# Kernel tuning notes

Measured on AMD Instinct MI355X. Metric: run time of the kernel, lower is better.

Reference implementation:

```python
import jax, jax.numpy as jnp
import numpy as np

B, N, F, E, D, H, L = 4, 2048, 2, 16, 32, 4, 2
GRAPH_LAYERS = 3
FLOW_ITERS = 10
COST_C = 1.0        # quadratic cost: c*x^2, inv_derivative(y) = y/(2c)
BIG_NUMBER = 1e7


def setup_inputs():
    key = jax.random.key(0)
    ks = jax.random.split(key, 20)
    node_features = jax.random.normal(ks[0], (B, N, F), jnp.float32)
    node_embeddings = jax.random.normal(ks[1], (B, N, E), jnp.float32)
    demands = jax.random.normal(ks[2], (B, N, 1), jnp.float32)
    demands = demands - demands.mean(axis=1, keepdims=True)  # flow conservation
    adj = (jax.random.uniform(ks[3], (B, N, N)) < 0.01).astype(jnp.float32)
    adj = adj * (1.0 - jnp.eye(N, dtype=jnp.float32))
    eye = jnp.broadcast_to(jnp.eye(N, dtype=jnp.float32), (B, N, N))
    neighborhoods = jnp.stack([eye, adj], axis=1)  # [B,L,N,N] hop-0 and hop-1
    def g(k, shape):
        return jax.random.normal(k, shape, jnp.float32) * 0.1
    params = {
        'We1': g(ks[4], (E + F, D)), 'be1': jnp.zeros((D,), jnp.float32),
        'We2': g(ks[5], (D, D)), 'be2': jnp.zeros((D,), jnp.float32),
        'w_attn': g(ks[6], (H, D)),
        'Wo': g(ks[7], (D, D)), 'bo': jnp.zeros((D,), jnp.float32),
        'Wz': g(ks[8], (D, D)), 'Uz': g(ks[9], (D, D)), 'bz': jnp.zeros((D,), jnp.float32),
        'Wr': g(ks[10], (D, D)), 'Ur': g(ks[11], (D, D)), 'br': jnp.zeros((D,), jnp.float32),
        'Wh': g(ks[12], (D, D)), 'Uh': g(ks[13], (D, D)), 'bh': jnp.zeros((D,), jnp.float32),
        'Wd1': g(ks[14], (D, D)), 'bd1': jnp.zeros((D,), jnp.float32),
        'Wd2': g(ks[15], (D, 1)), 'bd2': jnp.zeros((1,), jnp.float32),
        'Wv1': g(ks[16], (D, D)), 'bv1': jnp.zeros((D,), jnp.float32),
        'Wv2': g(ks[17], (D, 1)), 'bv2': jnp.zeros((1,), jnp.float32),
    }
    return {'node_features': node_features, 'node_embeddings': node_embeddings,
            'demands': demands, 'adj': adj, 'neighborhoods': neighborhoods, **params}


def _forward(node_features, node_embeddings, demands, adj, neighborhoods,
             We1, be1, We2, be2, w_attn, Wo, bo,
             Wz, Uz, bz, Wr, Ur, br, Wh, Uh, bh,
             Wd1, bd1, Wd2, bd2, Wv1, bv1, Wv2, bv2):
    # --- node encoder MLP (tanh, activate_final=True) ---
    x = jnp.concatenate([node_embeddings, node_features], axis=-1)   # [B,N,E+F]
    enc = jnp.tanh(jnp.tanh(x @ We1 + be1) @ We2 + be2)               # [B,N,D]
    # row-normalized neighborhood operators (degree-normalized aggregation)
    Mnorm = neighborhoods / (jnp.sum(neighborhoods, axis=-1, keepdims=True) + 1.0)
    # --- graph_layers x (attention neighborhood + GRU state update) ---
    for _ in range(GRAPH_LAYERS):
        agg = jnp.einsum('blnm,bmd->blnd', Mnorm, enc)                # [B,L,N,D]
        scores = jnp.einsum('blnd,hd->bhnl', jnp.tanh(agg), w_attn)   # [B,H,N,L]
        alpha = jax.nn.softmax(scores, axis=-1)
        ctx = jnp.einsum('bhnl,blnd->bnd', alpha, agg) / H            # mean over heads
        nbr = jnp.tanh(ctx @ Wo + bo)                                 # [B,N,D]
        z = jax.nn.sigmoid(nbr @ Wz + enc @ Uz + bz)
        r = jax.nn.sigmoid(nbr @ Wr + enc @ Ur + br)
        h = jnp.tanh(nbr @ Wh + (r * enc) @ Uh + bh)
        enc = z * enc + (1.0 - z) * h
    # --- primal: edge weights, masked softmax, proportional flow solver ---
    pred = (enc @ Wd1 + bd1) @ Wd2 + bd2                              # [B,N,1]
    pw = pred * jnp.transpose(pred, (0, 2, 1))                        # [B,N,N]
    weights = -BIG_NUMBER * (1.0 - adj) + pw
    fwp = jax.nn.softmax(weights, axis=-1)                            # rows sum to 1
    flow0 = fwp * jax.nn.relu(-demands)

    def step(flow, _):
        inflow = jnp.sum(flow, axis=1)[..., None]                     # [B,N,1]
        return fwp * jax.nn.relu(inflow - demands), None

    flow, _ = jax.lax.scan(step, flow0, None, length=FLOW_ITERS)
    flow_cost = jnp.sum(COST_C * flow * flow, axis=(1, 2))            # [B]
    # --- dual: dual variables, dual flows via inverse cost derivative ---
    dual = (enc @ Wv1 + bv1) @ Wv2 + bv2                              # [B,N,1]
    dd = dual - jnp.transpose(dual, (0, 2, 1))                        # [B,N,N]
    df = adj * jax.nn.relu(dd / (2.0 * COST_C))
    dual_cost = jnp.sum(COST_C * df * df - dd * df, axis=(1, 2)) \
        - jnp.sum(dual * demands, axis=(1, 2))                        # [B]
    return flow_cost - dual_cost                                      # primal-dual gap loss, [B]


def reference(node_features, node_embeddings, demands, adj, neighborhoods,
              We1, be1, We2, be2, w_attn, Wo, bo,
              Wz, Uz, bz, Wr, Ur, br, Wh, Uh, bh,
              Wd1, bd1, Wd2, bd2, Wv1, bv1, Wv2, bv2):
    return _forward(node_features, node_embeddings, demands, adj, neighborhoods,
                    We1, be1, We2, be2, w_attn, Wo, bo,
                    Wz, Uz, bz, Wr, Ur, br, Wh, Uh, bh,
                    Wd1, bd1, Wd2, bd2, Wv1, bv1, Wv2, bv2)
```

## Files before the change

kernel.cpp:

```cpp
#include <hip/hip_runtime.h>

#define NN 2048
#define NB 4
#define BN (NB * NN)
#define MAXD 96

__device__ __forceinline__ float fast_rcp(float x) { return __builtin_amdgcn_rcpf(x); }
__device__ __forceinline__ float fast_tanh(float x) {
    float a = __expf(2.0f * fabsf(x));
    float r = 1.0f - 2.0f * fast_rcp(1.0f + a);
    return copysignf(r, x);
}
__device__ __forceinline__ float fast_sigmoid(float x) {
    return fast_rcp(1.0f + __expf(-x));
}

__global__ __launch_bounds__(256) void k_front(
    const float* __restrict__ feat, const float* __restrict__ emb,
    const float* __restrict__ We1, const float* __restrict__ be1,
    const float* __restrict__ We2, const float* __restrict__ be2,
    float* __restrict__ enc_out,
    const float* __restrict__ adj, int* __restrict__ deg, int* __restrict__ cols,
    int* __restrict__ tdeg)
{
    int tid = threadIdx.x;
    if (blockIdx.x < 1024) {
        __shared__ float sW1[18 * 32], sb1[32], sW2[32 * 32], sb2[32];
        for (int i = tid; i < 18 * 32; i += 256) sW1[i] = We1[i];
        for (int i = tid; i < 32 * 32; i += 256) sW2[i] = We2[i];
        if (tid < 32) { sb1[tid] = be1[tid]; sb2[tid] = be2[tid]; }
        __syncthreads();
        int group = tid >> 5, j = tid & 31;
        int node = blockIdx.x * 8 + group;
        float x;
        if (j < 16)      x = emb[node * 16 + j];
        else if (j < 18) x = feat[node * 2 + (j - 16)];
        else             x = 0.f;
        float acc = sb1[j];
#pragma unroll
        for (int k = 0; k < 18; k++)
            acc += __shfl(x, k, 32) * sW1[k * 32 + j];
        float h = fast_tanh(acc);
        float acc2 = sb2[j];
#pragma unroll
        for (int k = 0; k < 32; k++)
            acc2 += __shfl(h, k, 32) * sW2[k * 32 + j];
        enc_out[node * 32 + j] = fast_tanh(acc2);
    } else {
        int wave = tid >> 6, lane = tid & 63;
        int row = (blockIdx.x - 1024) * 4 + wave;
        const float4* p = (const float4*)(adj + (size_t)row * NN);
        int cnt = 0;
        int base = row * MAXD;
#pragma unroll
        for (int it = 0; it < 8; it++) {
            float4 v = p[it * 64 + lane];
            float va[4] = { v.x, v.y, v.z, v.w };
#pragma unroll
            for (int c = 0; c < 4; c++) {
                unsigned long long m = __ballot(va[c] != 0.f);
                if (va[c] != 0.f) {
                    int pos = cnt + __popcll(m & ((1ull << lane) - 1ull));
                    if (pos < MAXD) cols[base + pos] = it * 256 + lane * 4 + c;
                }
                cnt += __popcll(m);
            }
        }
        if (lane == 0) {
            deg[row] = cnt < MAXD ? cnt : MAXD;
            tdeg[row] = 0;
        }
    }
}

__global__ __launch_bounds__(1024) void k_perm(
    const int* __restrict__ deg, const int* __restrict__ cols,
    int* __restrict__ perm, int* __restrict__ rank, int* __restrict__ degS)
{
    __shared__ int sIndeg[NN];
    __shared__ int sHist[MAXD + 1];
    __shared__ int sOff[MAXD + 1];
    int tid = threadIdx.x, b = blockIdx.x;
    for (int n = tid; n < NN; n += 1024) sIndeg[n] = 0;
    if (tid <= MAXD) sHist[tid] = 0;
    __syncthreads();
    for (int r = tid; r < NN; r += 1024) {
        int row = b * NN + r;
        int d = deg[row];
        const int* cp = cols + row * MAXD;
        for (int i = 0; i < d; i++) atomicAdd(&sIndeg[cp[i]], 1);
    }
    __syncthreads();
    for (int n = tid; n < NN; n += 1024) {
        int dg = sIndeg[n]; if (dg > MAXD) dg = MAXD;
        sIndeg[n] = dg;
        atomicAdd(&sHist[dg], 1);
    }
    __syncthreads();
    if (tid == 0) {
        int acc = 0;
        for (int i = 0; i <= MAXD; i++) { sOff[i] = acc; acc += sHist[i]; }
    }
    __syncthreads();
    for (int n = tid; n < NN; n += 1024) {
        int dg = sIndeg[n];
        int r = atomicAdd(&sOff[dg], 1);
        perm[b * NN + r] = n;
        rank[b * NN + n] = r;
        degS[b * NN + r] = dg;
    }
}

__device__ __forceinline__ float layer_rest(
    int g, int j, float e, float a1raw, int d,
    const float4* sPack, const float2* sWhUh, const float* sWo,
    const float* sAttn, const float* sbo, const float* sbz,
    const float* sbr, const float* sbh,
    float2 (*sNE)[32], float (*sCtx)[32])
{
    float agg0 = 0.5f * e;
    float a1 = a1raw * fast_rcp((float)(d + 1));
    float t0 = fast_tanh(agg0), t1 = fast_tanh(a1);
    float td = t0 - t1;
    float s0 = sAttn[j] * td, s1 = sAttn[32 + j] * td,
          s2 = sAttn[64 + j] * td, s3 = sAttn[96 + j] * td;
#pragma unroll
    for (int off = 16; off >= 1; off >>= 1) {
        s0 += __shfl_xor(s0, off, 32);
        s1 += __shfl_xor(s1, off, 32);
        s2 += __shfl_xor(s2, off, 32);
        s3 += __shfl_xor(s3, off, 32);
    }
    float c0 = 0.25f * (fast_sigmoid(s0) + fast_sigmoid(s1) +
                        fast_sigmoid(s2) + fast_sigmoid(s3));
    float ctx = c0 * agg0 + (1.0f - c0) * a1;
    sCtx[g][j] = ctx;
    float acc = sbo[j];
#pragma unroll
    for (int k = 0; k < 32; k += 2) {
        float2 c2 = *(const float2*)&sCtx[g][k];
        acc += c2.x * sWo[k * 32 + j] + c2.y * sWo[(k + 1) * 32 + j];
    }
    float nbr = fast_tanh(acc);
    sNE[g][j] = make_float2(nbr, e);
    float az = sbz[j], ar = sbr[j];
#pragma unroll
    for (int k = 0; k < 32; k += 2) {
        float4 ne2 = *(const float4*)&sNE[g][k];
        float4 w0  = sPack[k * 32 + j];
        float4 w1  = sPack[(k + 1) * 32 + j];
        az += ne2.x * w0.x + ne2.y * w0.y + ne2.z * w1.x + ne2.w * w1.y;
        ar += ne2.x * w0.z + ne2.y * w0.w + ne2.z * w1.z + ne2.w * w1.w;
    }
    float z = fast_sigmoid(az), r = fast_sigmoid(ar);
    sNE[g][j].y = r * e;
    float ah = sbh[j];
#pragma unroll
    for (int k = 0; k < 32; k += 2) {
        float4 ne2 = *(const float4*)&sNE[g][k];
        float2 w0 = sWhUh[k * 32 + j];
        float2 w1 = sWhUh[(k + 1) * 32 + j];
        ah += ne2.x * w0.x + ne2.y * w0.y + ne2.z * w1.x + ne2.w * w1.y;
    }
    float hc = fast_tanh(ah);
    return z * e + (1.0f - z) * hc;
}

__device__ __forceinline__ float hop1_gather(
    int g, int j, int d, const int* __restrict__ cp,
    const float* __restrict__ encB, int (*sCols)[64])
{
    sCols[g][j]      = cp[j];
    sCols[g][j + 32] = cp[j + 32];
    float a = 0.f, b = 0.f, c = 0.f, e4 = 0.f;
    int i = 0;
    for (; i + 3 < d; i += 4) {
        int m0 = sCols[g][i],     m1 = sCols[g][i + 1];
        int m2 = sCols[g][i + 2], m3 = sCols[g][i + 3];
        a  += encB[m0 * 32 + j];
        b  += encB[m1 * 32 + j];
        c  += encB[m2 * 32 + j];
        e4 += encB[m3 * 32 + j];
    }
    for (; i < d; i++) a += encB[sCols[g][i] * 32 + j];
    return (a + b) + (c + e4);
}

__global__ __launch_bounds__(1024) void k_layer(
    const float* __restrict__ enc_in, float* __restrict__ enc_out,
    const int* __restrict__ deg, const int* __restrict__ cols,
    const float* __restrict__ w_attn,
    const float* __restrict__ Wo, const float* __restrict__ bo,
    const float* __restrict__ Wz, const float* __restrict__ Uz, const float* __restrict__ bz,
    const float* __restrict__ Wr, const float* __restrict__ Ur, const float* __restrict__ br,
    const float* __restrict__ Wh, const float* __restrict__ Uh, const float* __restrict__ bh)
{
    __shared__ float4 sPack[1024];
    __shared__ float2 sWhUh[1024];
    __shared__ float  sWo[1024];
    __shared__ float  sAttn[128], sbo[32], sbz[32], sbr[32], sbh[32];
    __shared__ int    sCols[32][64];
    __shared__ __align__(16) float2 sNE[32][32];
    __shared__ __align__(16) float  sCtx[32][32];
    int tid = threadIdx.x;
    sPack[tid] = make_float4(Wz[tid], Uz[tid], Wr[tid], Ur[tid]);
    sWhUh[tid] = make_float2(Wh[tid], Uh[tid]);
    sWo[tid] = Wo[tid];
    if (tid < 128) sAttn[tid] = w_attn[tid];
    if (tid < 32) { sbo[tid] = bo[tid]; sbz[tid] = bz[tid]; sbr[tid] = br[tid]; sbh[tid] = bh[tid]; }
    int g = tid >> 5, j = tid & 31;
    int node = blockIdx.x * 32 + g;
    int b = node >> 11;
    const float* encB = enc_in + (size_t)(b * NN) * 32;
    float e = enc_in[node * 32 + j];
    int d = deg[node];
    const int* cp = cols + node * MAXD;
    float a1 = hop1_gather(g, j, d, cp, encB, sCols);
    __syncthreads();
    float eo = layer_rest(g, j, e, a1, d, sPack, sWhUh, sWo,
                          sAttn, sbo, sbz, sbr, sbh, sNE, sCtx);
    enc_out[node * 32 + j] = eo;
}

__global__ __launch_bounds__(1024) void k_layer_last(
    const float* __restrict__ enc_in,
    const int* __restrict__ deg, const int* __restrict__ cols,
    const float* __restrict__ w_attn,
    const float* __restrict__ Wo, const float* __restrict__ bo,
    const float* __restrict__ Wz, const float* __restrict__ Uz, const float* __restrict__ bz,
    const float* __restrict__ Wr, const float* __restrict__ Ur, const float* __restrict__ br,
    const float* __restrict__ Wh, const float* __restrict__ Uh, const float* __restrict__ bh,
    const float* __restrict__ Wd1, const float* __restrict__ bd1,
    const float* __restrict__ Wd2, const float* __restrict__ bd2,
    const float* __restrict__ Wv1, const float* __restrict__ bv1,
    const float* __restrict__ Wv2, const float* __restrict__ bv2,
    float* __restrict__ pred, float* __restrict__ dual)
{
    __shared__ float4 sPack[1024];
    __shared__ float2 sWhUh[1024];
    __shared__ float  sWo[1024];
    __shared__ float  sAttn[128], sbo[32], sbz[32], sbr[32], sbh[32];
    __shared__ float  swd[32], swv[32], shc[2];
    __shared__ int    sCols[32][64];
    __shared__ __align__(16) float2 sNE[32][32];
    __shared__ __align__(16) float  sCtx[32][32];
    int tid = threadIdx.x;
    sPack[tid] = make_float4(Wz[tid], Uz[tid], Wr[tid], Ur[tid]);
    sWhUh[tid] = make_float2(Wh[tid], Uh[tid]);
    sWo[tid] = Wo[tid];
    if (tid < 128) sAttn[tid] = w_attn[tid];
    if (tid < 32) { sbo[tid] = bo[tid]; sbz[tid] = bz[tid]; sbr[tid] = br[tid]; sbh[tid] = bh[tid]; }
    if (tid >= 64 && tid < 96) {
        int k = tid - 64;
        float a = 0.f, av = 0.f;
#pragma unroll
        for (int jj = 0; jj < 32; jj++) {
            a  += Wd1[k * 32 + jj] * Wd2[jj];
            av += Wv1[k * 32 + jj] * Wv2[jj];
        }
        swd[k] = a; swv[k] = av;
    }
    if (tid == 96) {
        float c1 = 0.f, c2 = 0.f;
#pragma unroll
        for (int jj = 0; jj < 32; jj++) {
            c1 += bd1[jj] * Wd2[jj];
            c2 += bv1[jj] * Wv2[jj];
        }
        shc[0] = c1 + bd2[0]; shc[1] = c2 + bv2[0];
    }
    int g = tid >> 5, j = tid & 31;
    int node = blockIdx.x * 32 + g;
    int b = node >> 11;
    const float* encB = enc_in + (size_t)(b * NN) * 32;
    float e = enc_in[node * 32 + j];
    int d = deg[node];
    const int* cp = cols + node * MAXD;
    float a1 = hop1_gather(g, j, d, cp, encB, sCols);
    __syncthreads();
    float eo = layer_rest(g, j, e, a1, d, sPack, sWhUh, sWo,
                          sAttn, sbo, sbz, sbr, sbh, sNE, sCtx);
    float pd = eo * swd[j];
    float dv = eo * swv[j];
#pragma unroll
    for (int off = 16; off >= 1; off >>= 1) {
        pd += __shfl_xor(pd, off, 32);
        dv += __shfl_xor(dv, off, 32);
    }
    if (j == 0) {
        pred[node] = pd + shc[0];
        dual[node] = dv + shc[1];
    }
}

__global__ __launch_bounds__(256) void k_edge_scatter(
    const int* __restrict__ deg, const int* __restrict__ cols,
    const float* __restrict__ pred, const float* __restrict__ dual,
    const int* __restrict__ rank,
    int* __restrict__ tdeg, unsigned* __restrict__ tpack,
    float* __restrict__ rowsq, float* __restrict__ rowdual)
{
    int wave = threadIdx.x >> 6, lane = threadIdx.x & 63;
    int row = blockIdx.x * 4 + wave;
    int b = row >> 11;
    int rloc = row & (NN - 1);
    const float* predB = pred + b * NN;
    const float* dualB = dual + b * NN;
    int d = deg[row];
    int base = row * MAXD;
    float pn = pred[row];
    float dn = dual[row];
    if (d <= 64) {
        int c = 0;
        float w = -1e30f, du = 0.f;
        bool act = lane < d;
        if (act) {
            c = cols[base + lane];
            w = pn * predB[c];
            float dd = dn - dualB[c];
            if (dd > 0.f) du = -0.25f * dd * dd;
        }
        float mx = w;
#pragma unroll
        for (int off = 32; off >= 1; off >>= 1) mx = fmaxf(mx, __shfl_xor(mx, off));
        float ex = act ? __expf(w - mx) : 0.f;
        float den = ex;
#pragma unroll
        for (int off = 32; off >= 1; off >>= 1) { den += __shfl_xor(den, off); du += __shfl_xor(du, off); }
        float f = ex * fast_rcp(den);
        float rs = f * f;
        if (act) {
            int pos = atomicAdd(&tdeg[b * NN + c], 1);
            if (pos < MAXD) {
                int rk = rank[b * NN + c];
                unsigned wv = ((__float_as_uint(f) + 0x400u) & 0xFFFFF800u) | (unsigned)rloc;
                tpack[(size_t)(b * MAXD + pos) * NN + rk] = wv;
            }
        } else rs = 0.f;
#pragma unroll
        for (int off = 32; off >= 1; off >>= 1) rs += __shfl_xor(rs, off);
        if (lane == 0) { rowsq[row] = rs; rowdual[row] = du; }
    } else {
        float mx = -1e30f;
        for (int i = lane; i < d; i += 64) {
            int c = cols[base + i];
            mx = fmaxf(mx, pn * predB[c]);
        }
#pragma unroll
        for (int off = 32; off >= 1; off >>= 1) mx = fmaxf(mx, __shfl_xor(mx, off));
        float den = 0.f, du = 0.f;
        for (int i = lane; i < d; i += 64) {
            int c = cols[base + i];
            den += __expf(pn * predB[c] - mx);
            float dd = dn - dualB[c];
            if (dd > 0.f) du -= 0.25f * dd * dd;
        }
#pragma unroll
        for (int off = 32; off >= 1; off >>= 1) { den += __shfl_xor(den, off); du += __shfl_xor(du, off); }
        float invden = fast_rcp(den);
        float rs = 0.f;
        for (int i = lane; i < d; i += 64) {
            int c = cols[base + i];
            float f = __expf(pn * predB[c] - mx) * invden;
            rs += f * f;
            int pos = atomicAdd(&tdeg[b * NN + c], 1);
            if (pos < MAXD) {
                int rk = rank[b * NN + c];
                unsigned wv = ((__float_as_uint(f) + 0x400u) & 0xFFFFF800u) | (unsigned)rloc;
                tpack[(size_t)(b * MAXD + pos) * NN + rk] = wv;
            }
        }
#pragma unroll
        for (int off = 32; off >= 1; off >>= 1) rs += __shfl_xor(rs, off);
        if (lane == 0) { rowsq[row] = rs; rowdual[row] = du; }
    }
}

__global__ __launch_bounds__(1024) void k_flow_batch(
    const int* __restrict__ perm, const int* __restrict__ degS,
    const unsigned* __restrict__ tpack,
    const float* __restrict__ demands,
    const float* __restrict__ rowsq, const float* __restrict__ rowdual,
    const float* __restrict__ dual, float* __restrict__ out)
{
    __shared__ float sdem[NN], sA[NN], sBuf[NN];
    __shared__ float red[3][16];
    int tid = threadIdx.x;
    int b = blockIdx.x;
    const float* demB = demands + b * NN;
    for (int n = tid; n < NN; n += 1024) {
        float dm = demB[n];
        sdem[n] = dm;
        sA[n] = fmaxf(-dm, 0.f);
    }
    __syncthreads();
    int q0 = tid, q1 = tid + 1024;
    int m0 = perm[b * NN + q0];
    int m1 = perm[b * NN + q1];
    int d0 = degS[b * NN + q0];
    int d1 = degS[b * NN + q1];
    float dm0 = sdem[m0], dm1 = sdem[m1];
    const unsigned* tp = tpack + (size_t)b * MAXD * NN;
#pragma unroll 1
    for (int it = 0; it < 5; it++) {
        {
            float a0 = 0.f, a1 = 0.f;
            for (int i = 0; i < d0; i++) {
                unsigned wv = tp[i * NN + q0];
                a0 += __uint_as_float(wv & 0xFFFFF800u) * sA[wv & 0x7FFu];
            }
            for (int i = 0; i < d1; i++) {
                unsigned wv = tp[i * NN + q1];
                a1 += __uint_as_float(wv & 0xFFFFF800u) * sA[wv & 0x7FFu];
            }
            sBuf[m0] = fmaxf(a0 - dm0, 0.f);
            sBuf[m1] = fmaxf(a1 - dm1, 0.f);
        }
        __syncthreads();
        {
            float a0 = 0.f, a1 = 0.f;
            for (int i = 0; i < d0; i++) {
                unsigned wv = tp[i * NN + q0];
                a0 += __uint_as_float(wv & 0xFFFFF800u) * sBuf[wv & 0x7FFu];
            }
            for (int i = 0; i < d1; i++) {
                unsigned wv = tp[i * NN + q1];
                a1 += __uint_as_float(wv & 0xFFFFF800u) * sBuf[wv & 0x7FFu];
            }
            sA[m0] = fmaxf(a0 - dm0, 0.f);
            sA[m1] = fmaxf(a1 - dm1, 0.f);
        }
        __syncthreads();
    }
    float fc = 0.f, ds = 0.f, dq = 0.f;
    for (int n = tid; n < NN; n += 1024) {
        int row = b * NN + n;
        float sv = sA[n];
        fc += rowsq[row] * sv * sv;
        ds += rowdual[row];
        dq += dual[row] * sdem[n];
    }
#pragma unroll
    for (int off = 32; off >= 1; off >>= 1) {
        fc += __shfl_xor(fc, off);
        ds += __shfl_xor(ds, off);
        dq += __shfl_xor(dq, off);
    }
    int wv = tid >> 6;
    if ((tid & 63) == 0) { red[0][wv] = fc; red[1][wv] = ds; red[2][wv] = dq; }
    __syncthreads();
    if (tid == 0) {
        float a = 0.f, s1 = 0.f, s2 = 0.f;
        for (int w = 0; w < 16; w++) { a += red[0][w]; s1 += red[1][w]; s2 += red[2][w]; }
        out[b] = a - s1 + s2;
    }
}

extern "C" void kernel_launch(void* const* d_in, const int* in_sizes, int n_in,
                              void* d_out, int out_size, void* d_ws, size_t ws_size,
                              hipStream_t stream) {
    const float* feat = (const float*)d_in[0];
    const float* emb  = (const float*)d_in[1];
    const float* dem  = (const float*)d_in[2];
    const float* adj  = (const float*)d_in[3];
    const float* We1 = (const float*)d_in[5];
    const float* be1 = (const float*)d_in[6];
    const float* We2 = (const float*)d_in[7];
    const float* be2 = (const float*)d_in[8];
    const float* w_attn = (const float*)d_in[9];
    const float* Wo = (const float*)d_in[10];
    const float* bo = (const float*)d_in[11];
    const float* Wz = (const float*)d_in[12];
    const float* Uz = (const float*)d_in[13];
    const float* bz = (const float*)d_in[14];
    const float* Wr = (const float*)d_in[15];
    const float* Ur = (const float*)d_in[16];
    const float* br = (const float*)d_in[17];
    const float* Wh = (const float*)d_in[18];
    const float* Uh = (const float*)d_in[19];
    const float* bh = (const float*)d_in[20];
    const float* Wd1 = (const float*)d_in[21];
    const float* bd1 = (const float*)d_in[22];
    const float* Wd2 = (const float*)d_in[23];
    const float* bd2 = (const float*)d_in[24];
    const float* Wv1 = (const float*)d_in[25];
    const float* bv1 = (const float*)d_in[26];
    const float* Wv2 = (const float*)d_in[27];
    const float* bv2 = (const float*)d_in[28];
    float* out = (float*)d_out;

    float* w = (float*)d_ws;
    float* enc0 = w;            w += (size_t)BN * 32;
    float* enc1 = w;            w += (size_t)BN * 32;
    int*   degp = (int*)w;      w += BN;
    int*   colp = (int*)w;      w += (size_t)BN * MAXD;
    float* pred = w;            w += BN;
    float* dual = w;            w += BN;
    float* rowsq = w;           w += BN;
    float* rowdual = w;         w += BN;
    int*   tdeg = (int*)w;      w += BN;
    int*   permp = (int*)w;     w += BN;
    int*   rankp = (int*)w;     w += BN;
    int*   degSp = (int*)w;     w += BN;
    unsigned* tpk = (unsigned*)w; w += (size_t)BN * MAXD;

    k_front<<<3072, 256, 0, stream>>>(feat, emb, We1, be1, We2, be2, enc0,
                                      adj, degp, colp, tdeg);
    k_perm<<<NB, 1024, 0, stream>>>(degp, colp, permp, rankp, degSp);
    k_layer<<<BN / 32, 1024, 0, stream>>>(enc0, enc1, degp, colp, w_attn,
                                          Wo, bo, Wz, Uz, bz, Wr, Ur, br, Wh, Uh, bh);
    k_layer<<<BN / 32, 1024, 0, stream>>>(enc1, enc0, degp, colp, w_attn,
                                          Wo, bo, Wz, Uz, bz, Wr, Ur, br, Wh, Uh, bh);
    k_layer_last<<<BN / 32, 1024, 0, stream>>>(enc0, degp, colp, w_attn,
                                               Wo, bo, Wz, Uz, bz, Wr, Ur, br, Wh, Uh, bh,
                                               Wd1, bd1, Wd2, bd2, Wv1, bv1, Wv2, bv2,
                                               pred, dual);
    k_edge_scatter<<<BN / 4, 256, 0, stream>>>(degp, colp, pred, dual, rankp,
                                               tdeg, tpk, rowsq, rowdual);
    k_flow_batch<<<NB, 1024, 0, stream>>>(permp, degSp, tpk, dem,
                                          rowsq, rowdual, dual, out);
}
```

Before: 399.8 us.

## Compute in-degrees with global atomics during adjacency compaction; simplify GRU loads

In-degree counting moves out of the single-block-per-batch k_perm kernel and into k_front's adjacency compaction pass, using global atomics on a buffer zeroed by a memset. k_perm then only builds the histogram and permutation, which removes the serial per-row loop over column lists that ran on just four blocks. The GRU and attention matvec loops in layer_rest drop the paired float4/float2 shared loads and the 16-byte alignment in favour of plain per-k loads. This adds global atomic traffic and an extra memset launch in exchange for a much shorter k_perm.

```diff
diff --git a/kernel.cpp b/kernel.cpp
--- a/kernel.cpp
+++ b/kernel.cpp
@@ -21,7 +21,7 @@
     const float* __restrict__ We2, const float* __restrict__ be2,
     float* __restrict__ enc_out,
     const float* __restrict__ adj, int* __restrict__ deg, int* __restrict__ cols,
-    int* __restrict__ tdeg)
+    int* __restrict__ tdeg, int* __restrict__ indeg)
 {
     int tid = threadIdx.x;
     if (blockIdx.x < 1024) {
@@ -49,6 +49,7 @@
     } else {
         int wave = tid >> 6, lane = tid & 63;
         int row = (blockIdx.x - 1024) * 4 + wave;
+        int b = row >> 11;
         const float4* p = (const float4*)(adj + (size_t)row * NN);
         int cnt = 0;
         int base = row * MAXD;
@@ -61,7 +62,11 @@
                 unsigned long long m = __ballot(va[c] != 0.f);
                 if (va[c] != 0.f) {
                     int pos = cnt + __popcll(m & ((1ull << lane) - 1ull));
-                    if (pos < MAXD) cols[base + pos] = it * 256 + lane * 4 + c;
+                    if (pos < MAXD) {
+                        int col = it * 256 + lane * 4 + c;
+                        cols[base + pos] = col;
+                        atomicAdd(&indeg[b * NN + col], 1);
+                    }
                 }
                 cnt += __popcll(m);
             }
@@ -74,40 +79,36 @@
 }
 
 __global__ __launch_bounds__(1024) void k_perm(
-    const int* __restrict__ deg, const int* __restrict__ cols,
+    const int* __restrict__ indeg,
     int* __restrict__ perm, int* __restrict__ rank, int* __restrict__ degS)
 {
-    __shared__ int sIndeg[NN];
     __shared__ int sHist[MAXD + 1];
     __shared__ int sOff[MAXD + 1];
     int tid = threadIdx.x, b = blockIdx.x;
-    for (int n = tid; n < NN; n += 1024) sIndeg[n] = 0;
     if (tid <= MAXD) sHist[tid] = 0;
     __syncthreads();
-    for (int r = tid; r < NN; r += 1024) {
-        int row = b * NN + r;
-        int d = deg[row];
-        const int* cp = cols + row * MAXD;
-        for (int i = 0; i < d; i++) atomicAdd(&sIndeg[cp[i]], 1);
-    }
-    __syncthreads();
-    for (int n = tid; n < NN; n += 1024) {
-        int dg = sIndeg[n]; if (dg > MAXD) dg = MAXD;
-        sIndeg[n] = dg;
-        atomicAdd(&sHist[dg], 1);
-    }
+    int dg0 = indeg[b * NN + tid];           if (dg0 > MAXD) dg0 = MAXD;
+    int dg1 = indeg[b * NN + tid + 1024];    if (dg1 > MAXD) dg1 = MAXD;
+    atomicAdd(&sHist[dg0], 1);
+    atomicAdd(&sHist[dg1], 1);
     __syncthreads();
     if (tid == 0) {
         int acc = 0;
         for (int i = 0; i <= MAXD; i++) { sOff[i] = acc; acc += sHist[i]; }
     }
     __syncthreads();
-    for (int n = tid; n < NN; n += 1024) {
-        int dg = sIndeg[n];
-        int r = atomicAdd(&sOff[dg], 1);
+    {
+        int r = atomicAdd(&sOff[dg0], 1);
+        perm[b * NN + r] = tid;
+        rank[b * NN + tid] = r;
+        degS[b * NN + r] = dg0;
+    }
+    {
+        int n = tid + 1024;
+        int r = atomicAdd(&sOff[dg1], 1);
         perm[b * NN + r] = n;
         rank[b * NN + n] = r;
-        degS[b * NN + r] = dg;
+        degS[b * NN + r] = dg1;
     }
 }
 
@@ -137,30 +138,26 @@
     sCtx[g][j] = ctx;
     float acc = sbo[j];
 #pragma unroll
-    for (int k = 0; k < 32; k += 2) {
-        float2 c2 = *(const float2*)&sCtx[g][k];
-        acc += c2.x * sWo[k * 32 + j] + c2.y * sWo[(k + 1) * 32 + j];
-    }
+    for (int k = 0; k < 32; k++)
+        acc += sCtx[g][k] * sWo[k * 32 + j];
     float nbr = fast_tanh(acc);
     sNE[g][j] = make_float2(nbr, e);
     float az = sbz[j], ar = sbr[j];
 #pragma unroll
-    for (int k = 0; k < 32; k += 2) {
-        float4 ne2 = *(const float4*)&sNE[g][k];
-        float4 w0  = sPack[k * 32 + j];
-        float4 w1  = sPack[(k + 1) * 32 + j];
-        az += ne2.x * w0.x + ne2.y * w0.y + ne2.z * w1.x + ne2.w * w1.y;
-        ar += ne2.x * w0.z + ne2.y * w0.w + ne2.z * w1.z + ne2.w * w1.w;
+    for (int k = 0; k < 32; k++) {
+        float2 ne = sNE[g][k];
+        float4 w  = sPack[k * 32 + j];
+        az += ne.x * w.x + ne.y * w.y;
+        ar += ne.x * w.z + ne.y * w.w;
     }
     float z = fast_sigmoid(az), r = fast_sigmoid(ar);
     sNE[g][j].y = r * e;
     float ah = sbh[j];
 #pragma unroll
-    for (int k = 0; k < 32; k += 2) {
-        float4 ne2 = *(const float4*)&sNE[g][k];
-        float2 w0 = sWhUh[k * 32 + j];
-        float2 w1 = sWhUh[(k + 1) * 32 + j];
-        ah += ne2.x * w0.x + ne2.y * w0.y + ne2.z * w1.x + ne2.w * w1.y;
+    for (int k = 0; k < 32; k++) {
+        float2 ne = sNE[g][k];
+        float2 wh = sWhUh[k * 32 + j];
+        ah += ne.x * wh.x + ne.y * wh.y;
     }
     float hc = fast_tanh(ah);
     return z * e + (1.0f - z) * hc;
@@ -200,8 +197,8 @@
     __shared__ float  sWo[1024];
     __shared__ float  sAttn[128], sbo[32], sbz[32], sbr[32], sbh[32];
     __shared__ int    sCols[32][64];
-    __shared__ __align__(16) float2 sNE[32][32];
-    __shared__ __align__(16) float  sCtx[32][32];
+    __shared__ float2 sNE[32][32];
+    __shared__ float  sCtx[32][32];
     int tid = threadIdx.x;
     sPack[tid] = make_float4(Wz[tid], Uz[tid], Wr[tid], Ur[tid]);
     sWhUh[tid] = make_float2(Wh[tid], Uh[tid]);
@@ -242,8 +239,8 @@
     __shared__ float  sAttn[128], sbo[32], sbz[32], sbr[32], sbh[32];
     __shared__ float  swd[32], swv[32], shc[2];
     __shared__ int    sCols[32][64];
-    __shared__ __align__(16) float2 sNE[32][32];
-    __shared__ __align__(16) float  sCtx[32][32];
+    __shared__ float2 sNE[32][32];
+    __shared__ float  sCtx[32][32];
     int tid = threadIdx.x;
     sPack[tid] = make_float4(Wz[tid], Uz[tid], Wr[tid], Ur[tid]);
     sWhUh[tid] = make_float2(Wh[tid], Uh[tid]);
@@ -499,14 +496,16 @@
     float* rowsq = w;           w += BN;
     float* rowdual = w;         w += BN;
     int*   tdeg = (int*)w;      w += BN;
+    int*   indegp = (int*)w;    w += BN;
     int*   permp = (int*)w;     w += BN;
     int*   rankp = (int*)w;     w += BN;
     int*   degSp = (int*)w;     w += BN;
     unsigned* tpk = (unsigned*)w; w += (size_t)BN * MAXD;
 
+    hipMemsetAsync(indegp, 0, BN * sizeof(int), stream);
     k_front<<<3072, 256, 0, stream>>>(feat, emb, We1, be1, We2, be2, enc0,
-                                      adj, degp, colp, tdeg);
-    k_perm<<<NB, 1024, 0, stream>>>(degp, colp, permp, rankp, degSp);
+                                      adj, degp, colp, tdeg, indegp);
+    k_perm<<<NB, 1024, 0, stream>>>(indegp, permp, rankp, degSp);
     k_layer<<<BN / 32, 1024, 0, stream>>>(enc0, enc1, degp, colp, w_attn,
                                           Wo, bo, Wz, Uz, bz, Wr, Ur, br, Wh, Uh, bh);
     k_layer<<<BN / 32, 1024, 0, stream>>>(enc1, enc0, degp, colp, w_attn,
```

New measurement: 384.9 us. -3.7%, faster.
